# Optimization experiments

Measured on AMD Instinct MI355X. Metric: run time of the kernel, lower is better.

## Reference

```python
import jax, jax.numpy as jnp
import numpy as np

GX, GY = 480, 360          # BEV grid (grid_size[0], grid_size[1])
C_OUT = 32                 # fea_compre
MAX_PT = 256               # max_pt_per_encode
NUM_VOX = GX * GY
BN_EPS = 1e-5


def setup_inputs() -> dict:
    key = jax.random.key(0)
    ks = jax.random.split(key, 12)
    B, N, F = 2, 100000, 7
    pt_fea = jax.random.normal(ks[0], (B, N, F), jnp.float32)
    xy_ind = jnp.stack([
        jax.random.randint(ks[1], (B, N), 0, GX),
        jax.random.randint(ks[2], (B, N), 0, GY),
    ], axis=-1).astype(jnp.int32)

    def lin(k, i, o):
        return 0.02 * jax.random.normal(k, (o, i), jnp.float32)

    inp = {"pt_fea": pt_fea, "xy_ind": xy_ind}
    dims = [(F, 64), (64, 128), (128, 256), (256, 512)]
    for j, (i, o) in enumerate(dims):
        inp[f"w{j}"] = lin(ks[3 + j], i, o)
        inp[f"b{j}"] = jnp.zeros((o,), jnp.float32)
    # BatchNorm (eval mode): bn0 on raw features, bn1..bn3 after linears 0..2
    for j, d in enumerate([F, 64, 128, 256]):
        inp[f"g{j}"] = jnp.ones((d,), jnp.float32)
        inp[f"be{j}"] = jnp.zeros((d,), jnp.float32)
        inp[f"m{j}"] = jnp.zeros((d,), jnp.float32)
        inp[f"v{j}"] = jnp.ones((d,), jnp.float32)
    inp["wc"] = lin(ks[7], 512, C_OUT)
    inp["bc"] = jnp.zeros((C_OUT,), jnp.float32)
    return inp


def _bn(x, g, b, m, v):
    return (x - m) * (g * jax.lax.rsqrt(v + BN_EPS)) + b


def reference(pt_fea, xy_ind,
              w0, b0, w1, b1, w2, b2, w3, b3,
              g0, be0, m0, v0, g1, be1, m1, v1,
              g2, be2, m2, v2, g3, be3, m3, v3,
              wc, bc):
    def pointnet(x):  # [N, 7] -> [N, 512]
        x = _bn(x, g0, be0, m0, v0)
        x = jax.nn.relu(_bn(x @ w0.T + b0, g1, be1, m1, v1))
        x = jax.nn.relu(_bn(x @ w1.T + b1, g2, be2, m2, v2))
        x = jax.nn.relu(_bn(x @ w2.T + b2, g3, be3, m3, v3))
        return x @ w3.T + b3

    def one_cloud(fea, xy):  # fea [N,7], xy [N,2] int
        N = fea.shape[0]
        vox = xy[:, 0] * GY + xy[:, 1]                      # linear voxel id
        # rank of each point within its voxel group (== grp_range_torch output)
        order = jnp.argsort(vox, stable=True)
        sid = vox[order]
        new_grp = jnp.concatenate([jnp.array([True]), sid[1:] != sid[:-1]])
        start = jax.lax.cummax(jnp.where(new_grp, jnp.arange(N), 0))
        rank_sorted = jnp.arange(N) - start
        rank = jnp.zeros((N,), rank_sorted.dtype).at[order].set(rank_sorted)
        remain = rank < MAX_PT                              # cap points per voxel

        pn = pointnet(fea)                                  # [N, 512]
        seg = jnp.where(remain, vox, NUM_VOX)               # dropped pts -> dummy seg
        maxf = jax.ops.segment_max(pn, seg, num_segments=NUM_VOX + 1)[:NUM_VOX]
        cnt = jax.ops.segment_sum(jnp.ones((N,), jnp.int32), seg,
                                  num_segments=NUM_VOX + 1)[:NUM_VOX]
        occ = (cnt > 0)[:, None]
        maxf = jnp.where(occ, maxf, 0.0)                    # kill -inf of empty voxels
        comp = jnp.where(occ, jax.nn.relu(maxf @ wc.T + bc), 0.0)  # [NUM_VOX, 32]
        return comp.reshape(GX, GY, C_OUT)

    grid = jax.vmap(one_cloud)(pt_fea, xy_ind)              # [B, GX, GY, 32]
    return jnp.transpose(grid, (0, 3, 1, 2))                # [B, 32, GX, GY]
```

## Files before the change

### kernel.cpp

```cpp
#include <hip/hip_runtime.h>

#define DEV __device__ __forceinline__

typedef _Float16 f16;
typedef __attribute__((ext_vector_type(8))) _Float16 half8;
typedef __attribute__((ext_vector_type(4))) _Float16 half4;
typedef __attribute__((ext_vector_type(4))) float floatx4;

constexpr int GXc = 480, GYc = 360;
constexpr int NVOX = GXc * GYc;
constexpr int BATCH = 2;
constexpr int NPT = 100000;
constexpr int FIN = 7;
constexpr int COUT = 32;
constexpr int MAXPT = 256;
constexpr float EPS = 1e-5f;
constexpr int NBLK = (NVOX + 255) / 256;
constexpr int FSTRIDE = NPT + 2;
constexpr int NB_PTS = (BATCH * NPT + 255) / 256;
constexpr int NB_FL  = (NPT + 255) / 256;

DEV unsigned f2ord(float f) {
  unsigned b = __float_as_uint(f);
  return (b & 0x80000000u) ? ~b : (b | 0x80000000u);
}
DEV float ord2f(unsigned u) {
  return __uint_as_float((u & 0x80000000u) ? (u & 0x7FFFFFFFu) : ~u);
}

__global__ __launch_bounds__(256)
void k_foldcount(const float* __restrict__ w0, const float* __restrict__ b0,
                 const float* __restrict__ w1, const float* __restrict__ b1,
                 const float* __restrict__ w2, const float* __restrict__ b2,
                 const float* __restrict__ w3, const float* __restrict__ wc,
                 const float* __restrict__ g0, const float* __restrict__ be0, const float* __restrict__ m0, const float* __restrict__ v0,
                 const float* __restrict__ g1, const float* __restrict__ be1, const float* __restrict__ m1, const float* __restrict__ v1,
                 const float* __restrict__ g2, const float* __restrict__ be2, const float* __restrict__ m2, const float* __restrict__ v2,
                 const float* __restrict__ g3, const float* __restrict__ be3, const float* __restrict__ m3, const float* __restrict__ v3,
                 float* __restrict__ A0, float* __restrict__ c0,
                 f16* __restrict__ A1h, float* __restrict__ c1,
                 f16* __restrict__ A2h, float* __restrict__ c2,
                 f16* __restrict__ W3h, f16* __restrict__ Wch,
                 const int* __restrict__ xy, int* __restrict__ vox, int* __restrict__ cnt)
{
  int blk = blockIdx.x;
  if (blk < 512) {
    int id = blk * 256 + threadIdx.x;
    if (id < 131072) W3h[id] = (f16)w3[id];
    if (id < 32768) { int m = id >> 7; A2h[id] = (f16)(w2[id] * (g3[m] * rsqrtf(v3[m] + EPS))); }
    if (id < 16384) Wch[id] = (f16)wc[id];
    if (id < 8192)  { int m = id >> 6; A1h[id] = (f16)(w1[id] * (g2[m] * rsqrtf(v2[m] + EPS))); }
    if (id < 512) {
      int m = id >> 3, k = id & 7;
      A0[id] = (k < 7) ? w0[m * 7 + k] * (g0[k] * rsqrtf(v0[k] + EPS)) * (g1[m] * rsqrtf(v1[m] + EPS)) : 0.f;
    }
    if (id < 64) {
      float t1m = g1[id] * rsqrtf(v1[id] + EPS);
      float a = b0[id];
      for (int k = 0; k < 7; k++) {
        float t0k = g0[k] * rsqrtf(v0[k] + EPS);
        a += (be0[k] - m0[k] * t0k) * w0[id * 7 + k];
      }
      c0[id] = (a - m1[id]) * t1m + be1[id];
    }
    if (id < 128) c1[id] = (b1[id] - m2[id]) * (g2[id] * rsqrtf(v2[id] + EPS)) + be2[id];
    if (id < 256) c2[id] = (b2[id] - m3[id]) * (g3[id] * rsqrtf(v3[id] + EPS)) + be3[id];
  } else {
    int id = (blk - 512) * 256 + threadIdx.x;
    if (id >= BATCH * NPT) return;
    int b = id / NPT;
    int x = xy[id * 2 + 0], y = xy[id * 2 + 1];
    int v = x * GYc + y;
    vox[id] = v;
    atomicAdd(&cnt[b * NVOX + v], 1);
  }
}

__global__ __launch_bounds__(256)
void k_scan1(const int* __restrict__ cnt, int* __restrict__ slot, int* __restrict__ pofs,
             unsigned long long* __restrict__ bsum)
{
  __shared__ unsigned long long sc[256];
  int g = blockIdx.x, tid = threadIdx.x;
  int b = g / NBLK, blk = g % NBLK;
  int v = blk * 256 + tid;
  int c = (v < NVOX) ? cnt[b * NVOX + v] : 0;
  unsigned long long val = ((unsigned long long)(c > 0 ? 1u : 0u) << 32) | (unsigned)c;
  sc[tid] = val;
  __syncthreads();
  for (int off = 1; off < 256; off <<= 1) {
    unsigned long long t = (tid >= off) ? sc[tid - off] : 0ull;
    __syncthreads();
    sc[tid] += t;
    __syncthreads();
  }
  if (v < NVOX) {
    unsigned long long e = sc[tid] - val;
    slot[b * NVOX + v] = (int)(e >> 32);
    pofs[b * NVOX + v] = (int)(unsigned)e;
  }
  if (tid == 255) bsum[g] = sc[255];
}

__global__ __launch_bounds__(256)
void k_scan2(const unsigned long long* __restrict__ bsum, unsigned long long* __restrict__ boff,
             int* __restrict__ Stot)
{
  __shared__ unsigned long long sc[256];
  int b = blockIdx.x, tid = threadIdx.x;
  unsigned long long run = 0;
  for (int i0 = 0; i0 < NBLK; i0 += 256) {
    int i = i0 + tid;
    unsigned long long val = (i < NBLK) ? bsum[b * NBLK + i] : 0ull;
    sc[tid] = val;
    __syncthreads();
    for (int off = 1; off < 256; off <<= 1) {
      unsigned long long t = (tid >= off) ? sc[tid - off] : 0ull;
      __syncthreads();
      sc[tid] += t;
      __syncthreads();
    }
    if (i < NBLK) boff[b * NBLK + i] = run + sc[tid] - val;
    run += sc[255];
    __syncthreads();
  }
  if (tid == 0) Stot[b] = (int)(run >> 32);
}

__global__ __launch_bounds__(256)
void k_scan3(const int* __restrict__ cnt, int* __restrict__ slot, int* __restrict__ pofs,
             const unsigned long long* __restrict__ boff, int* __restrict__ occv,
             int* __restrict__ flag)
{
  int g = blockIdx.x, tid = threadIdx.x;
  int b = g / NBLK, blk = g % NBLK;
  int v = blk * 256 + tid;
  if (v >= NVOX) return;
  unsigned long long bo = boff[g];
  int s = slot[b * NVOX + v] + (int)(bo >> 32);
  int pp = pofs[b * NVOX + v] + (int)(unsigned)bo;
  slot[b * NVOX + v] = s;
  pofs[b * NVOX + v] = pp;
  int c = cnt[b * NVOX + v];
  if (c > 0) {
    occv[b * NPT + s] = v;
    int use = (c > MAXPT) ? MAXPT : c;
    bool capped = (c > MAXPT);
    bool span = ((pp >> 2) != ((pp + use - 1) >> 2));
    if (span || capped) atomicOr(&flag[b * FSTRIDE + s], 1);
    if (capped) atomicOr(&flag[b * FSTRIDE + s + 1], 1);
  }
}

__global__ __launch_bounds__(256)
void k_postscan(const int* __restrict__ vox, const int* __restrict__ pofs,
                const int* __restrict__ slot, int* __restrict__ tmp,
                int* __restrict__ order, int* __restrict__ sgrp,
                const int* __restrict__ flag, const int* __restrict__ Stot,
                int* __restrict__ nflag, int* __restrict__ flaglist)
{
  int blk = blockIdx.x;
  if (blk < NB_PTS) {
    int id = blk * 256 + threadIdx.x;
    if (id >= BATCH * NPT) return;
    int b = id / NPT, p = id - b * NPT;
    int v = vox[id];
    int r = atomicAdd(&tmp[b * NVOX + v], 1);
    int pos = pofs[b * NVOX + v] + r;
    order[b * NPT + pos] = p;
    sgrp[b * NPT + pos] = (r < MAXPT) ? slot[b * NVOX + v] : -2;
  } else {
    int rb = blk - NB_PTS;
    int b = rb / NB_FL;
    int s = (rb % NB_FL) * 256 + threadIdx.x;
    if (s >= Stot[b]) return;
    if (flag[b * FSTRIDE + s]) {
      int i = atomicAdd(&nflag[b], 1);
      flaglist[b * NPT + i] = s;
    }
  }
}

__global__ __launch_bounds__(256)
void k_zero_flagged(unsigned* __restrict__ maxf, const int* __restrict__ flaglist,
                    const int* __restrict__ nflag, int b, int scap)
{
  long long n = (long long)nflag[b] * 128;
  uint4 z; z.x = z.y = z.z = z.w = 0u;
  long long stride = (long long)gridDim.x * 256;
  for (long long i = (long long)blockIdx.x * 256 + threadIdx.x; i < n; i += stride) {
    int s = flaglist[b * NPT + (int)(i >> 7)];
    if (s < scap) ((uint4*)(maxf + (size_t)s * 512))[i & 127] = z;
  }
}

__global__ __launch_bounds__(256)
void k_mlp012(const float* __restrict__ X, const int* __restrict__ order,
              const float* __restrict__ A0, const float* __restrict__ c0,
              const f16* __restrict__ A1h, const float* __restrict__ c1,
              const f16* __restrict__ A2h, const float* __restrict__ c2,
              f16* __restrict__ H3, int P)
{
  __shared__ __align__(16) char smem[65536];
  f16* H2s = (f16*)smem;
  f16* H1s = (f16*)(smem + 32768);
  f16* W1s = (f16*)(smem + 49152);
  float* A0s = (float*)smem;
  float* c0s = A0s + 512;
  f16* W2s = (f16*)(smem + 32768);

  const int tid = threadIdx.x;
  const int p0 = blockIdx.x * 128;
  const int wv = tid >> 6, ln = tid & 63;
  const int wp = (wv & 1) * 64, wm = (wv >> 1) * 64;
  const int l15 = ln & 15, lq = ln >> 4;

  A0s[tid] = A0[tid];
  A0s[tid + 256] = A0[tid + 256];
  if (tid < 64) c0s[tid] = c0[tid];
  #pragma unroll
  for (int it = 0; it < 4; it++) {
    int idx = it * 256 + tid;
    int r = idx >> 3, q = idx & 7;
    *(half8*)&W1s[r * 64 + (q ^ (r & 7)) * 8] = *(const half8*)(A1h + r * 64 + q * 8);
  }
  __syncthreads();

  {
    int p = tid >> 1, h = tid & 1;
    int pos = p0 + p; if (pos > P - 1) pos = P - 1;
    int pt = order[pos];
    float f[7];
    #pragma unroll
    for (int k = 0; k < 7; k++) f[k] = X[(size_t)pt * 7 + k];
    #pragma unroll
    for (int mm4 = 0; mm4 < 8; mm4++) {
      int mb = h * 32 + mm4 * 4;
      half4 ov;
      #pragma unroll
      for (int j = 0; j < 4; j++) {
        int m = mb + j;
        float a = c0s[m];
        #pragma unroll
        for (int k = 0; k < 7; k++) a += f[k] * A0s[m * 8 + k];
        ov[j] = (f16)(a > 0.f ? a : 0.f);
      }
      *(half4*)&H1s[p * 64 + ((mb >> 3) ^ (p & 7)) * 8 + (mb & 7)] = ov;
    }
  }
  __syncthreads();

  {
    floatx4 acc[4][4];
    #pragma unroll
    for (int i = 0; i < 4; i++)
      #pragma unroll
      for (int j = 0; j < 4; j++) acc[i][j] = (floatx4)0.f;
    #pragma unroll
    for (int k0 = 0; k0 < 64; k0 += 32) {
      half8 af[4], bf[4];
      #pragma unroll
      for (int i = 0; i < 4; i++) {
        int row = wp + i * 16 + l15;
        af[i] = *(const half8*)&H1s[row * 64 + (((k0 >> 3) + lq) ^ (row & 7)) * 8];
      }
      #pragma unroll
      for (int j = 0; j < 4; j++) {
        int row = wm + j * 16 + l15;
        bf[j] = *(const half8*)&W1s[row * 64 + (((k0 >> 3) + lq) ^ (row & 7)) * 8];
      }
      #pragma unroll
      for (int i = 0; i < 4; i++)
        #pragma unroll
        for (int j = 0; j < 4; j++)
          acc[i][j] = __builtin_amdgcn_mfma_f32_16x16x32_f16(af[i], bf[j], acc[i][j], 0, 0, 0);
    }
    float c1j[4];
    #pragma unroll
    for (int j = 0; j < 4; j++) c1j[j] = c1[wm + j * 16 + l15];
    #pragma unroll
    for (int i = 0; i < 4; i++) {
      #pragma unroll
      for (int r = 0; r < 4; r++) {
        int row = wp + i * 16 + lq * 4 + r;
        #pragma unroll
        for (int j = 0; j < 4; j++) {
          int col = wm + j * 16 + l15;
          float v = acc[i][j][r] + c1j[j];
          if (v < 0.f) v = 0.f;
          H2s[row * 128 + ((col >> 3) ^ (row & 7)) * 8 + (col & 7)] = (f16)v;
        }
      }
    }
  }
  __syncthreads();

  for (int mc = 0; mc < 2; mc++) {
    floatx4 acc[4][4];
    #pragma unroll
    for (int i = 0; i < 4; i++)
      #pragma unroll
      for (int j = 0; j < 4; j++) acc[i][j] = (floatx4)0.f;
    for (int k0 = 0; k0 < 128; k0 += 32) {
      __syncthreads();
      #pragma unroll
      for (int it = 0; it < 2; it++) {
        int idx = it * 256 + tid;
        int r = idx >> 2, q = idx & 3;
        *(half8*)&W2s[r * 40 + q * 8] =
            *(const half8*)(A2h + (size_t)(mc * 128 + r) * 128 + k0 + q * 8);
      }
      __syncthreads();
      half8 af[4], bf[4];
      #pragma unroll
      for (int i = 0; i < 4; i++) {
        int row = wp + i * 16 + l15;
        af[i] = *(const half8*)&H2s[row * 128 + (((k0 >> 3) + lq) ^ (row & 7)) * 8];
      }
      #pragma unroll
      for (int j = 0; j < 4; j++)
        bf[j] = *(const half8*)&W2s[(wm + j * 16 + l15) * 40 + lq * 8];
      #pragma unroll
      for (int i = 0; i < 4; i++)
        #pragma unroll
        for (int j = 0; j < 4; j++)
          acc[i][j] = __builtin_amdgcn_mfma_f32_16x16x32_f16(af[i], bf[j], acc[i][j], 0, 0, 0);
    }
    float c2j[4];
    #pragma unroll
    for (int j = 0; j < 4; j++) c2j[j] = c2[mc * 128 + wm + j * 16 + l15];
    #pragma unroll
    for (int i = 0; i < 4; i++) {
      #pragma unroll
      for (int r = 0; r < 4; r++) {
        int prow = p0 + wp + i * 16 + lq * 4 + r;
        if (prow < P) {
          #pragma unroll
          for (int j = 0; j < 4; j++) {
            int col = mc * 128 + wm + j * 16 + l15;
            float v = acc[i][j][r] + c2j[j];
            if (v < 0.f) v = 0.f;
            H3[(size_t)prow * 256 + col] = (f16)v;
          }
        }
      }
    }
  }
}

constexpr int LW = 40;

__global__ __launch_bounds__(256)
void k_gemm16_smax(const f16* __restrict__ A, const f16* __restrict__ W,
                   const float* __restrict__ bias, int P,
                   unsigned* __restrict__ maxf, const int* __restrict__ sg,
                   int chunk0, int rest, int scap)
{
  constexpr int K = 256, M = 512;
  __shared__ f16 Xs[128 * LW];
  __shared__ f16 Ws[128 * LW];
  const int tid = threadIdx.x;
  const int p0 = blockIdx.x * 128;
  const int m0 = blockIdx.y * 128;
  const int wv = tid >> 6, ln = tid & 63;
  const int wp = (wv & 1) * 64, wm = (wv >> 1) * 64;
  const int l15 = ln & 15, lq = ln >> 4;

  floatx4 acc[4][4];
  #pragma unroll
  for (int i = 0; i < 4; i++)
    #pragma unroll
    for (int j = 0; j < 4; j++) acc[i][j] = (floatx4)0.f;

  const int sr = tid >> 2, sq = tid & 3;
  for (int k0 = 0; k0 < K; k0 += 32) {
    {
      int pr = p0 + sr; if (pr > P - 1) pr = P - 1;
      *(half8*)&Xs[sr * LW + sq * 8] = *(const half8*)(A + (size_t)pr * K + k0 + sq * 8);
      *(half8*)&Ws[sr * LW + sq * 8] = *(const half8*)(W + (size_t)(m0 + sr) * K + k0 + sq * 8);
      int r2 = sr + 64;
      int pr2 = p0 + r2; if (pr2 > P - 1) pr2 = P - 1;
      *(half8*)&Xs[r2 * LW + sq * 8] = *(const half8*)(A + (size_t)pr2 * K + k0 + sq * 8);
      *(half8*)&Ws[r2 * LW + sq * 8] = *(const half8*)(W + (size_t)(m0 + r2) * K + k0 + sq * 8);
    }
    __syncthreads();
    half8 af[4], bf[4];
    #pragma unroll
    for (int i = 0; i < 4; i++)
      af[i] = *(const half8*)&Xs[(wp + i * 16 + l15) * LW + lq * 8];
    #pragma unroll
    for (int j = 0; j < 4; j++)
      bf[j] = *(const half8*)&Ws[(wm + j * 16 + l15) * LW + lq * 8];
    #pragma unroll
    for (int i = 0; i < 4; i++)
      #pragma unroll
      for (int j = 0; j < 4; j++)
        acc[i][j] = __builtin_amdgcn_mfma_f32_16x16x32_f16(af[i], bf[j], acc[i][j], 0, 0, 0);
    __syncthreads();
  }

  float bj[4];
  #pragma unroll
  for (int j = 0; j < 4; j++) bj[j] = bias[m0 + wm + j * 16 + l15];
  const int cbase = m0 + wm + l15;

  #pragma unroll
  for (int i = 0; i < 4; i++) {
    int pr0 = p0 + wp + i * 16 + lq * 4;
    float run[4];
    int gcur = -1;
    bool openL = false;

    auto flushrun = [&](int gc, bool open) {
      if (gc >= scap) return;
      unsigned* row = maxf + (size_t)gc * M + cbase;
      if (open) {
        #pragma unroll
        for (int j = 0; j < 4; j++) atomicMax(row + j * 16, f2ord(run[j]));
      } else {
        #pragma unroll
        for (int j = 0; j < 4; j++) row[j * 16] = f2ord(run[j]);
      }
    };

    int glast = (chunk0 + pr0 > 0) ? sg[pr0 - 1] : -1;
    #pragma unroll
    for (int r = 0; r < 4; r++) {
      int pos = pr0 + r;
      int g = (pos < P) ? sg[pos] : -1;
      if (g >= 0) {
        if (g == gcur) {
          #pragma unroll
          for (int j = 0; j < 4; j++) run[j] = fmaxf(run[j], acc[i][j][r] + bj[j]);
        } else {
          if (gcur >= 0) flushrun(gcur, openL);
          gcur = g;
          openL = (glast == g) || (glast == -2);
          #pragma unroll
          for (int j = 0; j < 4; j++) run[j] = acc[i][j][r] + bj[j];
        }
      } else {
        if (gcur >= 0) { flushrun(gcur, openL || (g == -2)); gcur = -1; }
      }
      glast = g;
    }
    if (gcur >= 0) {
      int gnext = (pr0 + 4 < rest) ? sg[pr0 + 4] : -1;
      flushrun(gcur, openL || (gnext == gcur) || (gnext == -2));
    }
  }
}

__global__ __launch_bounds__(256)
void k_compress_mfma(const unsigned* __restrict__ maxf, const f16* __restrict__ Wch,
                     const float* __restrict__ bc, const int* __restrict__ Stot,
                     float* __restrict__ outc, int scap)
{
  int S = Stot[0]; if (S > scap) S = scap;
  const int s0 = blockIdx.x * 128;
  if (s0 >= S) return;
  __shared__ f16 Xs[128 * LW];
  __shared__ f16 Wcs[32 * LW];
  const int tid = threadIdx.x;
  const int wv = tid >> 6, ln = tid & 63;
  const int l15 = ln & 15, lq = ln >> 4;

  floatx4 acc[2][2];
  #pragma unroll
  for (int i = 0; i < 2; i++)
    #pragma unroll
    for (int j = 0; j < 2; j++) acc[i][j] = (floatx4)0.f;

  for (int k0 = 0; k0 < 512; k0 += 32) {
    #pragma unroll
    for (int l = 0; l < 4; l++) {
      int idx = l * 256 + tid;
      int r = idx >> 3, q = idx & 7;
      int srow = s0 + r; if (srow > S - 1) srow = S - 1;
      uint4 uv = *(const uint4*)(maxf + (size_t)srow * 512 + k0 + q * 4);
      half4 hv;
      hv[0] = (f16)ord2f(uv.x); hv[1] = (f16)ord2f(uv.y);
      hv[2] = (f16)ord2f(uv.z); hv[3] = (f16)ord2f(uv.w);
      *(half4*)&Xs[r * LW + q * 4] = hv;
    }
    {
      int c = tid >> 3, q = tid & 7;
      *(half4*)&Wcs[c * LW + q * 4] = *(const half4*)(Wch + (size_t)c * 512 + k0 + q * 4);
    }
    __syncthreads();
    half8 af[2], bf[2];
    #pragma unroll
    for (int i = 0; i < 2; i++)
      af[i] = *(const half8*)&Xs[(wv * 32 + i * 16 + l15) * LW + lq * 8];
    #pragma unroll
    for (int j = 0; j < 2; j++)
      bf[j] = *(const half8*)&Wcs[(j * 16 + l15) * LW + lq * 8];
    #pragma unroll
    for (int i = 0; i < 2; i++)
      #pragma unroll
      for (int j = 0; j < 2; j++)
        acc[i][j] = __builtin_amdgcn_mfma_f32_16x16x32_f16(af[i], bf[j], acc[i][j], 0, 0, 0);
    __syncthreads();
  }

  #pragma unroll
  for (int i = 0; i < 2; i++) {
    int sb = s0 + wv * 32 + i * 16 + lq * 4;
    #pragma unroll
    for (int r = 0; r < 4; r++) {
      int s = sb + r;
      if (s < S) {
        #pragma unroll
        for (int j = 0; j < 2; j++) {
          int c = j * 16 + l15;
          float v = acc[i][j][r] + bc[c];
          outc[(size_t)s * COUT + c] = v > 0.f ? v : 0.f;
        }
      }
    }
  }
}

__global__ __launch_bounds__(256)
void k_scatter_out(const float* __restrict__ outc, const int* __restrict__ cnt,
                   const int* __restrict__ slot, float* __restrict__ outb, int scap)
{
  int v = blockIdx.x * 256 + threadIdx.x;
  if (v >= NVOX) return;
  bool occ = cnt[v] > 0;
  int s = slot[v];
  float4 a[8];
  if (occ && s < scap) {
    #pragma unroll
    for (int q = 0; q < 8; q++) a[q] = *(const float4*)(outc + (size_t)s * COUT + q * 4);
  } else {
    #pragma unroll
    for (int q = 0; q < 8; q++) { a[q].x = 0.f; a[q].y = 0.f; a[q].z = 0.f; a[q].w = 0.f; }
  }
  const float* af = (const float*)a;
  #pragma unroll
  for (int c = 0; c < 32; c++) outb[(size_t)c * NVOX + v] = af[c];
}

extern "C" void kernel_launch(void* const* d_in, const int* in_sizes, int n_in,
                              void* d_out, int out_size, void* d_ws, size_t ws_size,
                              hipStream_t stream) {
  (void)in_sizes; (void)n_in; (void)out_size;
  const float* pt_fea = (const float*)d_in[0];
  const int*   xy     = (const int*)d_in[1];
  const float* w0 = (const float*)d_in[2];  const float* b0 = (const float*)d_in[3];
  const float* w1 = (const float*)d_in[4];  const float* b1 = (const float*)d_in[5];
  const float* w2 = (const float*)d_in[6];  const float* b2 = (const float*)d_in[7];
  const float* w3 = (const float*)d_in[8];  const float* b3 = (const float*)d_in[9];
  const float* g0 = (const float*)d_in[10]; const float* be0 = (const float*)d_in[11];
  const float* m0 = (const float*)d_in[12]; const float* v0  = (const float*)d_in[13];
  const float* g1 = (const float*)d_in[14]; const float* be1 = (const float*)d_in[15];
  const float* m1 = (const float*)d_in[16]; const float* v1  = (const float*)d_in[17];
  const float* g2 = (const float*)d_in[18]; const float* be2 = (const float*)d_in[19];
  const float* m2 = (const float*)d_in[20]; const float* v2  = (const float*)d_in[21];
  const float* g3 = (const float*)d_in[22]; const float* be3 = (const float*)d_in[23];
  const float* m3 = (const float*)d_in[24]; const float* v3  = (const float*)d_in[25];
  const float* wc = (const float*)d_in[26]; const float* bc = (const float*)d_in[27];
  float* outp = (float*)d_out;

  char* base = (char*)d_ws;
  size_t off = 0;
  auto alloc = [&](size_t n) -> void* {
    void* p = base + off;
    off = (off + n + 255) & ~(size_t)255;
    return p;
  };
  float* A0f = (float*)alloc(512 * 4);    float* c0f = (float*)alloc(64 * 4);
  f16* A1h = (f16*)alloc(8192 * 2);       float* c1f = (float*)alloc(128 * 4);
  f16* A2h = (f16*)alloc(32768 * 2);      float* c2f = (float*)alloc(256 * 4);
  f16* W3h = (f16*)alloc(131072 * 2);
  f16* Wch = (f16*)alloc(16384 * 2);
  int* vox  = (int*)alloc((size_t)BATCH * NPT * 4);
  int* slot = (int*)alloc((size_t)BATCH * NVOX * 4);
  int* pofs = (int*)alloc((size_t)BATCH * NVOX * 4);
  unsigned long long* bsum = (unsigned long long*)alloc((size_t)BATCH * NBLK * 8);
  unsigned long long* boff = (unsigned long long*)alloc((size_t)BATCH * NBLK * 8);
  int* Stot = (int*)alloc((size_t)BATCH * 4);
  int* occv = (int*)alloc((size_t)BATCH * NPT * 4);
  int* order = (int*)alloc((size_t)BATCH * NPT * 4);
  int* sgrp  = (int*)alloc((size_t)BATCH * NPT * 4);
  int* flist = (int*)alloc((size_t)BATCH * NPT * 4);
  float* outc = (float*)alloc((size_t)NPT * COUT * 4);
  size_t zoff0 = off;
  int* cnt  = (int*)alloc((size_t)BATCH * NVOX * 4);
  int* tmp  = (int*)alloc((size_t)BATCH * NVOX * 4);
  int* flag = (int*)alloc((size_t)BATCH * FSTRIDE * 4);
  int* nflag = (int*)alloc((size_t)BATCH * 4);
  size_t zlen = off - zoff0;

  int scap = NPT;
  size_t remain = (ws_size > off) ? ws_size - off : 0;
  size_t minH = (size_t)128 * 256 * 2;
  if (remain < (size_t)scap * 512 * 4 + minH) {
    size_t avail = (remain > minH) ? remain - minH : 0;
    scap = (int)(avail / 2048);
    if (scap < 1) scap = 1;
  }
  unsigned* maxf = (unsigned*)alloc((size_t)scap * 512 * 4);

  size_t hrem = (ws_size > off) ? ws_size - off : 0;
  int P = (int)((hrem / ((size_t)256 * 2)) & ~(size_t)127);
  if (P > NPT) P = ((NPT + 127) / 128) * 128;
  if (P < 128) P = 128;
  f16* H3 = (f16*)alloc((size_t)P * 256 * 2);

  hipMemsetAsync(base + zoff0, 0, zlen, stream);

  k_foldcount<<<512 + NB_PTS, 256, 0, stream>>>(w0, b0, w1, b1, w2, b2, w3, wc,
                                                g0, be0, m0, v0, g1, be1, m1, v1,
                                                g2, be2, m2, v2, g3, be3, m3, v3,
                                                A0f, c0f, A1h, c1f, A2h, c2f, W3h, Wch,
                                                xy, vox, cnt);
  k_scan1<<<BATCH * NBLK, 256, 0, stream>>>(cnt, slot, pofs, bsum);
  k_scan2<<<BATCH, 256, 0, stream>>>(bsum, boff, Stot);
  k_scan3<<<BATCH * NBLK, 256, 0, stream>>>(cnt, slot, pofs, boff, occv, flag);
  k_postscan<<<NB_PTS + BATCH * NB_FL, 256, 0, stream>>>(vox, pofs, slot, tmp, order, sgrp,
                                                         flag, Stot, nflag, flist);

  for (int b = 0; b < BATCH; b++) {
    k_zero_flagged<<<128, 256, 0, stream>>>(maxf, flist, nflag, b, scap);
    for (int p0 = 0; p0 < NPT; p0 += P) {
      int pc = (NPT - p0 < P) ? (NPT - p0) : P;
      k_mlp012<<<(pc + 127) / 128, 256, 0, stream>>>(pt_fea + (size_t)b * NPT * FIN,
                                                     order + (size_t)b * NPT + p0,
                                                     A0f, c0f, A1h, c1f, A2h, c2f,
                                                     H3, pc);
      dim3 gC((pc + 127) / 128, 4);
      k_gemm16_smax<<<gC, 256, 0, stream>>>(H3, W3h, b3, pc,
                                            maxf, sgrp + (size_t)b * NPT + p0,
                                            p0, NPT - p0, scap);
    }
    k_compress_mfma<<<(NPT + 127) / 128, 256, 0, stream>>>(maxf, Wch, bc, Stot + b,
                                                           outc, scap);
    k_scatter_out<<<(NVOX + 255) / 256, 256, 0, stream>>>(outc, cnt + (size_t)b * NVOX,
                                                          slot + (size_t)b * NVOX,
                                                          outp + (size_t)b * COUT * NVOX,
                                                          scap);
  }
}
```

Baseline: 573.3 us.

## Store voxel max buffer as fp16 and keep full weight tiles in LDS

```diff
diff --git a/kernel.cpp b/kernel.cpp
--- a/kernel.cpp
+++ b/kernel.cpp
@@ -20,12 +20,21 @@
 constexpr int NB_PTS = (BATCH * NPT + 255) / 256;
 constexpr int NB_FL  = (NPT + 255) / 256;
 
-DEV unsigned f2ord(float f) {
-  unsigned b = __float_as_uint(f);
-  return (b & 0x80000000u) ? ~b : (b | 0x80000000u);
-}
-DEV float ord2f(unsigned u) {
-  return __uint_as_float((u & 0x80000000u) ? (u & 0x7FFFFFFFu) : ~u);
+DEV void atom_max_f16(f16* p, float v) {
+  unsigned* word = (unsigned*)((size_t)p & ~(size_t)3);
+  const int hi = ((size_t)p >> 1) & 1;
+  const unsigned short nb = __builtin_bit_cast(unsigned short, (f16)v);
+  unsigned old = *(volatile unsigned*)word;
+  while (true) {
+    unsigned short cb = hi ? (unsigned short)(old >> 16) : (unsigned short)(old & 0xFFFFu);
+    f16 cf = __builtin_bit_cast(f16, cb);
+    if ((float)cf >= v) return;
+    unsigned neww = hi ? ((old & 0x0000FFFFu) | ((unsigned)nb << 16))
+                       : ((old & 0xFFFF0000u) | (unsigned)nb);
+    unsigned got = atomicCAS(word, old, neww);
+    if (got == old) return;
+    old = got;
+  }
 }
 
 __global__ __launch_bounds__(256)
@@ -182,15 +191,15 @@
 }
 
 __global__ __launch_bounds__(256)
-void k_zero_flagged(unsigned* __restrict__ maxf, const int* __restrict__ flaglist,
+void k_zero_flagged(f16* __restrict__ maxf, const int* __restrict__ flaglist,
                     const int* __restrict__ nflag, int b, int scap)
 {
-  long long n = (long long)nflag[b] * 128;
-  uint4 z; z.x = z.y = z.z = z.w = 0u;
+  long long n = (long long)nflag[b] * 64;
+  uint4 z; z.x = z.y = z.z = z.w = 0xFC00FC00u;
   long long stride = (long long)gridDim.x * 256;
   for (long long i = (long long)blockIdx.x * 256 + threadIdx.x; i < n; i += stride) {
-    int s = flaglist[b * NPT + (int)(i >> 7)];
-    if (s < scap) ((uint4*)(maxf + (size_t)s * 512))[i & 127] = z;
+    int s = flaglist[b * NPT + (int)(i >> 6)];
+    if (s < scap) ((uint4*)(maxf + (size_t)s * 512))[i & 63] = z;
   }
 }
 
@@ -348,17 +357,14 @@
   }
 }
 
-constexpr int LW = 40;
-
 __global__ __launch_bounds__(256)
 void k_gemm16_smax(const f16* __restrict__ A, const f16* __restrict__ W,
                    const float* __restrict__ bias, int P,
-                   unsigned* __restrict__ maxf, const int* __restrict__ sg,
+                   f16* __restrict__ maxf, const int* __restrict__ sg,
                    int chunk0, int rest, int scap)
 {
   constexpr int K = 256, M = 512;
-  __shared__ f16 Xs[128 * LW];
-  __shared__ f16 Ws[128 * LW];
+  __shared__ f16 Ws[128 * 256];
   const int tid = threadIdx.x;
   const int p0 = blockIdx.x * 128;
   const int m0 = blockIdx.y * 128;
@@ -366,37 +372,46 @@
   const int wp = (wv & 1) * 64, wm = (wv >> 1) * 64;
   const int l15 = ln & 15, lq = ln >> 4;
 
+  #pragma unroll
+  for (int it = 0; it < 16; it++) {
+    int idx = it * 256 + tid;
+    int row = idx >> 5, oct = idx & 31;
+    *(half8*)&Ws[row * 256 + (oct >> 3) * 64 + ((oct & 7) ^ (row & 7)) * 8] =
+        *(const half8*)(W + (size_t)(m0 + row) * K + oct * 8);
+  }
+
+  const f16* arow[4];
+  #pragma unroll
+  for (int i = 0; i < 4; i++) {
+    int r = p0 + wp + i * 16 + l15; if (r > P - 1) r = P - 1;
+    arow[i] = A + (size_t)r * K;
+  }
+
   floatx4 acc[4][4];
   #pragma unroll
   for (int i = 0; i < 4; i++)
     #pragma unroll
     for (int j = 0; j < 4; j++) acc[i][j] = (floatx4)0.f;
 
-  const int sr = tid >> 2, sq = tid & 3;
+  __syncthreads();
+
   for (int k0 = 0; k0 < K; k0 += 32) {
-    {
-      int pr = p0 + sr; if (pr > P - 1) pr = P - 1;
-      *(half8*)&Xs[sr * LW + sq * 8] = *(const half8*)(A + (size_t)pr * K + k0 + sq * 8);
-      *(half8*)&Ws[sr * LW + sq * 8] = *(const half8*)(W + (size_t)(m0 + sr) * K + k0 + sq * 8);
-      int r2 = sr + 64;
-      int pr2 = p0 + r2; if (pr2 > P - 1) pr2 = P - 1;
-      *(half8*)&Xs[r2 * LW + sq * 8] = *(const half8*)(A + (size_t)pr2 * K + k0 + sq * 8);
-      *(half8*)&Ws[r2 * LW + sq * 8] = *(const half8*)(W + (size_t)(m0 + r2) * K + k0 + sq * 8);
-    }
-    __syncthreads();
     half8 af[4], bf[4];
     #pragma unroll
     for (int i = 0; i < 4; i++)
-      af[i] = *(const half8*)&Xs[(wp + i * 16 + l15) * LW + lq * 8];
-    #pragma unroll
-    for (int j = 0; j < 4; j++)
-      bf[j] = *(const half8*)&Ws[(wm + j * 16 + l15) * LW + lq * 8];
+      af[i] = *(const half8*)(arow[i] + k0 + lq * 8);
+    int oct = (k0 >> 3) + lq;
+    int hi64 = (oct >> 3) * 64, lo = oct & 7;
+    #pragma unroll
+    for (int j = 0; j < 4; j++) {
+      int row = wm + j * 16 + l15;
+      bf[j] = *(const half8*)&Ws[row * 256 + hi64 + (lo ^ (row & 7)) * 8];
+    }
     #pragma unroll
     for (int i = 0; i < 4; i++)
       #pragma unroll
       for (int j = 0; j < 4; j++)
         acc[i][j] = __builtin_amdgcn_mfma_f32_16x16x32_f16(af[i], bf[j], acc[i][j], 0, 0, 0);
-    __syncthreads();
   }
 
   float bj[4];
@@ -413,13 +428,13 @@
 
     auto flushrun = [&](int gc, bool open) {
       if (gc >= scap) return;
-      unsigned* row = maxf + (size_t)gc * M + cbase;
+      f16* row = maxf + (size_t)gc * M + cbase;
       if (open) {
         #pragma unroll
-        for (int j = 0; j < 4; j++) atomicMax(row + j * 16, f2ord(run[j]));
+        for (int j = 0; j < 4; j++) atom_max_f16(row + j * 16, run[j]);
       } else {
         #pragma unroll
-        for (int j = 0; j < 4; j++) row[j * 16] = f2ord(run[j]);
+        for (int j = 0; j < 4; j++) row[j * 16] = (f16)run[j];
       }
     };
 
@@ -452,55 +467,58 @@
 }
 
 __global__ __launch_bounds__(256)
-void k_compress_mfma(const unsigned* __restrict__ maxf, const f16* __restrict__ Wch,
+void k_compress_mfma(const f16* __restrict__ maxf, const f16* __restrict__ Wch,
                      const float* __restrict__ bc, const int* __restrict__ Stot,
                      float* __restrict__ outc, int scap)
 {
   int S = Stot[0]; if (S > scap) S = scap;
   const int s0 = blockIdx.x * 128;
   if (s0 >= S) return;
-  __shared__ f16 Xs[128 * LW];
-  __shared__ f16 Wcs[32 * LW];
+  __shared__ f16 Wcs[32 * 512];
   const int tid = threadIdx.x;
   const int wv = tid >> 6, ln = tid & 63;
   const int l15 = ln & 15, lq = ln >> 4;
 
+  #pragma unroll
+  for (int it = 0; it < 8; it++) {
+    int idx = it * 256 + tid;
+    int row = idx >> 6, oct = idx & 63;
+    *(half8*)&Wcs[row * 512 + (oct >> 3) * 64 + ((oct & 7) ^ (row & 7)) * 8] =
+        *(const half8*)(Wch + (size_t)row * 512 + oct * 8);
+  }
+
+  const f16* arow[2];
+  #pragma unroll
+  for (int i = 0; i < 2; i++) {
+    int r = s0 + wv * 32 + i * 16 + l15; if (r > S - 1) r = S - 1;
+    arow[i] = maxf + (size_t)r * 512;
+  }
+
   floatx4 acc[2][2];
   #pragma unroll
   for (int i = 0; i < 2; i++)
     #pragma unroll
     for (int j = 0; j < 2; j++) acc[i][j] = (floatx4)0.f;
 
+  __syncthreads();
+
   for (int k0 = 0; k0 < 512; k0 += 32) {
-    #pragma unroll
-    for (int l = 0; l < 4; l++) {
-      int idx = l * 256 + tid;
-      int r = idx >> 3, q = idx & 7;
-      int srow = s0 + r; if (srow > S - 1) srow = S - 1;
-      uint4 uv = *(const uint4*)(maxf + (size_t)srow * 512 + k0 + q * 4);
-      half4 hv;
-      hv[0] = (f16)ord2f(uv.x); hv[1] = (f16)ord2f(uv.y);
-      hv[2] = (f16)ord2f(uv.z); hv[3] = (f16)ord2f(uv.w);
-      *(half4*)&Xs[r * LW + q * 4] = hv;
-    }
-    {
-      int c = tid >> 3, q = tid & 7;
-      *(half4*)&Wcs[c * LW + q * 4] = *(const half4*)(Wch + (size_t)c * 512 + k0 + q * 4);
-    }
-    __syncthreads();
     half8 af[2], bf[2];
     #pragma unroll
     for (int i = 0; i < 2; i++)
-      af[i] = *(const half8*)&Xs[(wv * 32 + i * 16 + l15) * LW + lq * 8];
-    #pragma unroll
-    for (int j = 0; j < 2; j++)
-      bf[j] = *(const half8*)&Wcs[(j * 16 + l15) * LW + lq * 8];
+      af[i] = *(const half8*)(arow[i] + k0 + lq * 8);
+    int oct = (k0 >> 3) + lq;
+    int hi64 = (oct >> 3) * 64, lo = oct & 7;
+    #pragma unroll
+    for (int j = 0; j < 2; j++) {
+      int row = j * 16 + l15;
+      bf[j] = *(const half8*)&Wcs[row * 512 + hi64 + (lo ^ (row & 7)) * 8];
+    }
     #pragma unroll
     for (int i = 0; i < 2; i++)
       #pragma unroll
       for (int j = 0; j < 2; j++)
         acc[i][j] = __builtin_amdgcn_mfma_f32_16x16x32_f16(af[i], bf[j], acc[i][j], 0, 0, 0);
-    __syncthreads();
   }
 
   #pragma unroll
@@ -596,12 +614,12 @@
   int scap = NPT;
   size_t remain = (ws_size > off) ? ws_size - off : 0;
   size_t minH = (size_t)128 * 256 * 2;
-  if (remain < (size_t)scap * 512 * 4 + minH) {
+  if (remain < (size_t)scap * 512 * 2 + minH) {
     size_t avail = (remain > minH) ? remain - minH : 0;
-    scap = (int)(avail / 2048);
+    scap = (int)(avail / 1024);
     if (scap < 1) scap = 1;
   }
-  unsigned* maxf = (unsigned*)alloc((size_t)scap * 512 * 4);
+  f16* maxf = (f16*)alloc((size_t)scap * 512 * 2);
 
   size_t hrem = (ws_size > off) ? ws_size - off : 0;
   int P = (int)((hrem / ((size_t)256 * 2)) & ~(size_t)127);
```

Result: slower. 959.0 us (+67.3%).

## Store per-voxel max features in fp16 and stage exclusive writes through LDS

Applied to the files above, without the earlier changes.

```diff
diff --git a/kernel.cpp b/kernel.cpp
--- a/kernel.cpp
+++ b/kernel.cpp
@@ -20,12 +20,21 @@
 constexpr int NB_PTS = (BATCH * NPT + 255) / 256;
 constexpr int NB_FL  = (NPT + 255) / 256;
 
-DEV unsigned f2ord(float f) {
-  unsigned b = __float_as_uint(f);
-  return (b & 0x80000000u) ? ~b : (b | 0x80000000u);
-}
-DEV float ord2f(unsigned u) {
-  return __uint_as_float((u & 0x80000000u) ? (u & 0x7FFFFFFFu) : ~u);
+DEV void atom_max_f16(f16* p, float v) {
+  unsigned* word = (unsigned*)((size_t)p & ~(size_t)3);
+  const int hi = ((size_t)p >> 1) & 1;
+  const unsigned short nb = __builtin_bit_cast(unsigned short, (f16)v);
+  unsigned old = *(volatile unsigned*)word;
+  while (true) {
+    unsigned short cb = hi ? (unsigned short)(old >> 16) : (unsigned short)(old & 0xFFFFu);
+    f16 cf = __builtin_bit_cast(f16, cb);
+    if ((float)cf >= v) return;
+    unsigned neww = hi ? ((old & 0x0000FFFFu) | ((unsigned)nb << 16))
+                       : ((old & 0xFFFF0000u) | (unsigned)nb);
+    unsigned got = atomicCAS(word, old, neww);
+    if (got == old) return;
+    old = got;
+  }
 }
 
 __global__ __launch_bounds__(256)
@@ -182,15 +191,15 @@
 }
 
 __global__ __launch_bounds__(256)
-void k_zero_flagged(unsigned* __restrict__ maxf, const int* __restrict__ flaglist,
+void k_zero_flagged(f16* __restrict__ maxf, const int* __restrict__ flaglist,
                     const int* __restrict__ nflag, int b, int scap)
 {
-  long long n = (long long)nflag[b] * 128;
-  uint4 z; z.x = z.y = z.z = z.w = 0u;
+  long long n = (long long)nflag[b] * 64;
+  uint4 z; z.x = z.y = z.z = z.w = 0xFC00FC00u;
   long long stride = (long long)gridDim.x * 256;
   for (long long i = (long long)blockIdx.x * 256 + threadIdx.x; i < n; i += stride) {
-    int s = flaglist[b * NPT + (int)(i >> 7)];
-    if (s < scap) ((uint4*)(maxf + (size_t)s * 512))[i & 127] = z;
+    int s = flaglist[b * NPT + (int)(i >> 6)];
+    if (s < scap) ((uint4*)(maxf + (size_t)s * 512))[i & 63] = z;
   }
 }
 
@@ -353,12 +362,16 @@
 __global__ __launch_bounds__(256)
 void k_gemm16_smax(const f16* __restrict__ A, const f16* __restrict__ W,
                    const float* __restrict__ bias, int P,
-                   unsigned* __restrict__ maxf, const int* __restrict__ sg,
+                   f16* __restrict__ maxf, const int* __restrict__ sg,
                    int chunk0, int rest, int scap)
 {
   constexpr int K = 256, M = 512;
-  __shared__ f16 Xs[128 * LW];
-  __shared__ f16 Ws[128 * LW];
+  __shared__ __align__(16) char smem[33536];
+  f16* Xs = (f16*)smem;
+  f16* Ws = (f16*)(smem + 128 * LW * 2);
+  f16* Cs = (f16*)smem;
+  int* grow = (int*)(smem + 32768);
+
   const int tid = threadIdx.x;
   const int p0 = blockIdx.x * 128;
   const int m0 = blockIdx.y * 128;
@@ -399,6 +412,9 @@
     __syncthreads();
   }
 
+  if (tid < 128) grow[tid] = -1;
+  __syncthreads();
+
   float bj[4];
   #pragma unroll
   for (int j = 0; j < 4; j++) bj[j] = bias[m0 + wm + j * 16 + l15];
@@ -407,19 +423,21 @@
   #pragma unroll
   for (int i = 0; i < 4; i++) {
     int pr0 = p0 + wp + i * 16 + lq * 4;
+    int lr0 = wp + i * 16 + lq * 4;
     float run[4];
-    int gcur = -1;
+    int gcur = -1, rstart = 0;
     bool openL = false;
 
-    auto flushrun = [&](int gc, bool open) {
+    auto flushrun = [&](int gc, bool open, int lrs) {
       if (gc >= scap) return;
-      unsigned* row = maxf + (size_t)gc * M + cbase;
       if (open) {
+        f16* row = maxf + (size_t)gc * M + cbase;
         #pragma unroll
-        for (int j = 0; j < 4; j++) atomicMax(row + j * 16, f2ord(run[j]));
+        for (int j = 0; j < 4; j++) atom_max_f16(row + j * 16, run[j]);
       } else {
         #pragma unroll
-        for (int j = 0; j < 4; j++) row[j * 16] = f2ord(run[j]);
+        for (int j = 0; j < 4; j++) Cs[lrs * 128 + wm + j * 16 + l15] = (f16)run[j];
+        if (l15 == 0) grow[lrs] = gc;
       }
     };
 
@@ -433,26 +451,36 @@
           #pragma unroll
           for (int j = 0; j < 4; j++) run[j] = fmaxf(run[j], acc[i][j][r] + bj[j]);
         } else {
-          if (gcur >= 0) flushrun(gcur, openL);
-          gcur = g;
+          if (gcur >= 0) flushrun(gcur, openL, lr0 + rstart);
+          gcur = g; rstart = r;
           openL = (glast == g) || (glast == -2);
           #pragma unroll
           for (int j = 0; j < 4; j++) run[j] = acc[i][j][r] + bj[j];
         }
       } else {
-        if (gcur >= 0) { flushrun(gcur, openL || (g == -2)); gcur = -1; }
+        if (gcur >= 0) { flushrun(gcur, openL || (g == -2), lr0 + rstart); gcur = -1; }
       }
       glast = g;
     }
     if (gcur >= 0) {
       int gnext = (pr0 + 4 < rest) ? sg[pr0 + 4] : -1;
-      flushrun(gcur, openL || (gnext == gcur) || (gnext == -2));
-    }
-  }
-}
-
-__global__ __launch_bounds__(256)
-void k_compress_mfma(const unsigned* __restrict__ maxf, const f16* __restrict__ Wch,
+      flushrun(gcur, openL || (gnext == gcur) || (gnext == -2), lr0 + rstart);
+    }
+  }
+  __syncthreads();
+
+  {
+    int lane16 = tid & 15;
+    for (int lr = tid >> 4; lr < 128; lr += 16) {
+      int g = grow[lr];
+      if (g >= 0 && g < scap)
+        *(half8*)(maxf + (size_t)g * M + m0 + lane16 * 8) = *(half8*)&Cs[lr * 128 + lane16 * 8];
+    }
+  }
+}
+
+__global__ __launch_bounds__(256)
+void k_compress_mfma(const f16* __restrict__ maxf, const f16* __restrict__ Wch,
                      const float* __restrict__ bc, const int* __restrict__ Stot,
                      float* __restrict__ outc, int scap)
 {
@@ -473,15 +501,11 @@
 
   for (int k0 = 0; k0 < 512; k0 += 32) {
     #pragma unroll
-    for (int l = 0; l < 4; l++) {
+    for (int l = 0; l < 2; l++) {
       int idx = l * 256 + tid;
-      int r = idx >> 3, q = idx & 7;
+      int r = idx >> 2, q = idx & 3;
       int srow = s0 + r; if (srow > S - 1) srow = S - 1;
-      uint4 uv = *(const uint4*)(maxf + (size_t)srow * 512 + k0 + q * 4);
-      half4 hv;
-      hv[0] = (f16)ord2f(uv.x); hv[1] = (f16)ord2f(uv.y);
-      hv[2] = (f16)ord2f(uv.z); hv[3] = (f16)ord2f(uv.w);
-      *(half4*)&Xs[r * LW + q * 4] = hv;
+      *(half8*)&Xs[r * LW + q * 8] = *(const half8*)(maxf + (size_t)srow * 512 + k0 + q * 8);
     }
     {
       int c = tid >> 3, q = tid & 7;
@@ -596,12 +620,12 @@
   int scap = NPT;
   size_t remain = (ws_size > off) ? ws_size - off : 0;
   size_t minH = (size_t)128 * 256 * 2;
-  if (remain < (size_t)scap * 512 * 4 + minH) {
+  if (remain < (size_t)scap * 512 * 2 + minH) {
     size_t avail = (remain > minH) ? remain - minH : 0;
-    scap = (int)(avail / 2048);
+    scap = (int)(avail / 1024);
     if (scap < 1) scap = 1;
   }
-  unsigned* maxf = (unsigned*)alloc((size_t)scap * 512 * 4);
+  f16* maxf = (f16*)alloc((size_t)scap * 512 * 2);
 
   size_t hrem = (ws_size > off) ? ws_size - off : 0;
   int P = (int)((hrem / ((size_t)256 * 2)) & ~(size_t)127);
```

Result: slower. 789.4 us (+37.7%).
